# Optimization experiments

Measured on AMD Instinct MI355X. Metric: run time of the kernel, lower is better.

Reference implementation:

```python
import jax, jax.numpy as jnp
import numpy as np

B, K, V = 64, 8, 128000
PLACEHOLDER = -1


def setup_inputs() -> dict:
    key = jax.random.key(0)
    k1, k2, k3, k4, k5 = jax.random.split(key, 5)
    draft_token_ids = jax.random.randint(k1, (B, K), 0, V, dtype=jnp.int32)
    # normalized probability distributions, as the kernel expects
    draft_probs = jax.nn.softmax(jax.random.normal(k2, (B, K, V), dtype=jnp.float32), axis=-1)
    target_probs = jax.nn.softmax(jax.random.normal(k3, (B, K, V), dtype=jnp.float32), axis=-1)
    bonus_token_ids = jax.random.randint(k4, (B,), 0, V, dtype=jnp.int32)
    uniform_samples = jax.random.uniform(k5, (B, K), dtype=jnp.float32)
    return {
        "draft_token_ids": draft_token_ids,
        "draft_probs": draft_probs,
        "target_probs": target_probs,
        "bonus_token_ids": bonus_token_ids,
        "uniform_samples": uniform_samples,
    }


def reference(draft_token_ids, draft_probs, target_probs, bonus_token_ids, uniform_samples):
    """Speculative-decoding rejection sampling (dense layout, all requests have K drafts).

    Returns (output_token_ids [B,K+1] int32, num_accepted, accepted_counts,
             recovered_counts, bonus_counts) matching RejectionSampleOutput.
    """
    b_idx = jnp.arange(B)
    # gather p(t), q(t) at the drafted token ids: [B, K]
    p = jnp.take_along_axis(target_probs, draft_token_ids[..., None].astype(jnp.int32), axis=-1)[..., 0]
    q = jnp.take_along_axis(draft_probs, draft_token_ids[..., None].astype(jnp.int32), axis=-1)[..., 0]
    accept_prob = jnp.minimum(1.0, p / jnp.maximum(q, 1e-10))
    accept = uniform_samples < accept_prob                      # [B, K] bool
    # number of leading accepted tokens (sequential accept/reject chain)
    prefix = jnp.cumprod(accept.astype(jnp.int32), axis=1)
    num_acc = jnp.sum(prefix, axis=1)                           # [B]
    all_acc = num_acc == K
    # first rejected position (clamped for the all-accepted case)
    j = jnp.minimum(num_acc, K - 1)
    tgt_j = target_probs[b_idx, j]                              # [B, V]
    drf_j = draft_probs[b_idx, j]                               # [B, V]
    # recovery distribution: normalized max(p - q, 0); sample via inverse-CDF
    res = jnp.maximum(tgt_j - drf_j, 0.0)
    cdf = jnp.cumsum(res, axis=-1)                              # [B, V]
    total = cdf[:, -1]
    u_j = uniform_samples[b_idx, j]
    recovered = jnp.argmax(cdf > (u_j * total)[:, None], axis=-1)
    recovered = jnp.where(total > 0, recovered, jnp.argmax(tgt_j, axis=-1)).astype(jnp.int32)
    # last emitted token: bonus if everything accepted, else recovered
    last = jnp.where(all_acc, bonus_token_ids, recovered)       # [B]
    pos = jnp.arange(K + 1)[None, :]                            # [1, K+1]
    draft_pad = jnp.pad(draft_token_ids, ((0, 0), (0, 1)))      # [B, K+1]
    out = jnp.where(pos < num_acc[:, None], draft_pad,
                    jnp.where(pos == num_acc[:, None], last[:, None], PLACEHOLDER))
    accepted_counts = num_acc.astype(jnp.int32)
    recovered_counts = (1 - all_acc.astype(jnp.int32))
    bonus_counts = all_acc.astype(jnp.int32)
    return (out.astype(jnp.int32), num_acc.astype(jnp.int32), accepted_counts,
            recovered_counts, bonus_counts)
```

## Files before the change

### kernel.cpp

```cpp
#include <hip/hip_runtime.h>

#define BB 64
#define KK 8
#define VV 128000
#define TILE 1024
#define NTILES 125
#define SPLIT 8
#define TPS 16
#define NWAVES 8
#define PLACEHOLDER (-1)

#define WS_TSUM 0
#define WS_AV   (BB * NTILES)
#define WS_AI   (WS_AV + BB * SPLIT * NWAVES)
#define WS_NA   (WS_AI + BB * SPLIT * NWAVES)

__device__ __forceinline__ int accept_na(const int* __restrict__ draft_ids,
                                         const float* __restrict__ draft_probs,
                                         const float* __restrict__ target_probs,
                                         const float* __restrict__ uniforms, int b) {
    int   ids[KK];
    float us[KK], ps[KK], qs[KK];
#pragma unroll
    for (int k = 0; k < KK; ++k) ids[k] = draft_ids[b * KK + k];
#pragma unroll
    for (int k = 0; k < KK; ++k) us[k] = uniforms[b * KK + k];
#pragma unroll
    for (int k = 0; k < KK; ++k) {
        long r = (long)(b * KK + k) * VV + ids[k];
        ps[k]  = target_probs[r];
        qs[k]  = draft_probs[r];
    }
    int  na  = 0;
    bool run = true;
#pragma unroll
    for (int k = 0; k < KK; ++k) {
        bool acc = us[k] < fminf(1.0f, ps[k] / fmaxf(qs[k], 1e-10f));
        run      = run && acc;
        na += run ? 1 : 0;
    }
    return na;
}

__global__ __launch_bounds__(512) void pass_a_kernel(
    const int* __restrict__ draft_ids, const float* __restrict__ draft_probs,
    const float* __restrict__ target_probs, const float* __restrict__ uniforms,
    float* __restrict__ ws_f, int* __restrict__ ws_i) {
    const int s    = blockIdx.x;
    const int b    = blockIdx.y;
    const int tid  = threadIdx.x;
    const int lane = tid & 63;
    const int w    = tid >> 6;

    int na = accept_na(draft_ids, draft_probs, target_probs, uniforms, b);
    if (s == 0 && tid == 0) ws_i[WS_NA + b] = na;
    if (na == KK) return;
    int j = na < (KK - 1) ? na : (KK - 1);

    const float* __restrict__ tgt = target_probs + (long)(b * KK + j) * VV;
    const float* __restrict__ drf = draft_probs + (long)(b * KK + j) * VV;

    float mval = -1.0f;
    int   midx = 0;
    const int t0 = s * TPS;
#pragma unroll
    for (int i = 0; i < 2; ++i) {
        int t = t0 + w + NWAVES * i;
        if (t >= NTILES) continue;
        float ssum = 0.0f;
#pragma unroll
        for (int g = 0; g < 4; ++g) {
            int    off = t * TILE + g * 256 + lane * 4;
            float4 tv  = *(const float4*)(tgt + off);
            float4 dv  = *(const float4*)(drf + off);
            ssum += fmaxf(tv.x - dv.x, 0.0f) + fmaxf(tv.y - dv.y, 0.0f) +
                    fmaxf(tv.z - dv.z, 0.0f) + fmaxf(tv.w - dv.w, 0.0f);
            if (tv.x > mval) { mval = tv.x; midx = off; }
            if (tv.y > mval) { mval = tv.y; midx = off + 1; }
            if (tv.z > mval) { mval = tv.z; midx = off + 2; }
            if (tv.w > mval) { mval = tv.w; midx = off + 3; }
        }
        for (int o = 32; o > 0; o >>= 1) ssum += __shfl_xor(ssum, o, 64);
        if (lane == 0) ws_f[WS_TSUM + b * NTILES + t] = ssum;
    }
    for (int o = 32; o > 0; o >>= 1) {
        float ov = __shfl_xor(mval, o, 64);
        int   oi = __shfl_xor(midx, o, 64);
        if (ov > mval || (ov == mval && oi < midx)) { mval = ov; midx = oi; }
    }
    if (lane == 0) {
        ws_f[WS_AV + b * SPLIT * NWAVES + s * NWAVES + w] = mval;
        ws_i[WS_AI + b * SPLIT * NWAVES + s * NWAVES + w] = midx;
    }
}

__global__ __launch_bounds__(64) void finalize_kernel(
    const int* __restrict__ draft_ids, const float* __restrict__ draft_probs,
    const float* __restrict__ target_probs, const int* __restrict__ bonus_ids,
    const float* __restrict__ uniforms, const float* __restrict__ ws_f,
    const int* __restrict__ ws_i, int* __restrict__ out) {
    const int b    = blockIdx.x;
    const int lane = threadIdx.x;

    __shared__ float s_ts[NTILES];
    __shared__ float s_total, s_thr, s_P;
    __shared__ int   s_ct;

    float ts0 = ws_f[WS_TSUM + b * NTILES + lane];
    float ts1 = 0.0f;
    if (lane < NTILES - 64) ts1 = ws_f[WS_TSUM + b * NTILES + lane + 64];

    int na  = ws_i[WS_NA + b];
    int all = (na == KK) ? 1 : 0;
    int j   = na < (KK - 1) ? na : (KK - 1);

    if (lane <= KK) {
        bool wr = true;
        int  v;
        if (lane < na) v = draft_ids[b * KK + lane];
        else if (lane == na) { if (all) v = bonus_ids[b]; else wr = false; }
        else v = PLACEHOLDER;
        if (wr) out[b * (KK + 1) + lane] = v;
    }
    if (lane == 0) {
        out[BB * (KK + 1) + b]          = na;
        out[BB * (KK + 1) + BB + b]     = na;
        out[BB * (KK + 1) + 2 * BB + b] = 1 - all;
        out[BB * (KK + 1) + 3 * BB + b] = all;
    }
    if (all) return;

    s_ts[lane] = ts0;
    if (lane < NTILES - 64) s_ts[lane + 64] = ts1;
    __syncthreads();

    if (lane == 0) {
        float u_j   = uniforms[b * KK + j];
        float total = 0.0f;
        for (int t = 0; t < NTILES; ++t) total += s_ts[t];
        float thr = u_j * total;
        float run = 0.0f;
        int   ct  = -1;
        float P   = 0.0f;
        for (int t = 0; t < NTILES; ++t) {
            if (run + s_ts[t] > thr) { ct = t; P = run; break; }
            run += s_ts[t];
        }
        s_total = total; s_thr = thr; s_P = P; s_ct = ct;
    }
    __syncthreads();

    const float total = s_total, thr = s_thr, P = s_P;
    const int   ct    = s_ct;
    int rec;
    if (total > 0.0f) {
        if (ct < 0) {
            rec = VV - 1;
        } else {
            const float* __restrict__ tgt = target_probs + (long)(b * KK + j) * VV;
            const float* __restrict__ drf = draft_probs + (long)(b * KK + j) * VV;
            float G     = 0.0f;
            int   cand  = 0x7fffffff;
            int   tbase = ct * TILE;
#pragma unroll
            for (int g = 0; g < 4; ++g) {
                int    off = tbase + g * 256 + lane * 4;
                float4 tv  = *(const float4*)(tgt + off);
                float4 dv  = *(const float4*)(drf + off);
                float  r0  = fmaxf(tv.x - dv.x, 0.0f);
                float  r1  = fmaxf(tv.y - dv.y, 0.0f);
                float  r2  = fmaxf(tv.z - dv.z, 0.0f);
                float  r3  = fmaxf(tv.w - dv.w, 0.0f);
                float  ls  = r0 + r1 + r2 + r3;
                float  inc = ls;
                for (int o = 1; o < 64; o <<= 1) {
                    float n = __shfl_up(inc, o, 64);
                    if (lane >= o) inc += n;
                }
                float lex  = inc - ls;
                float runp = P + G + lex;
                float p0 = runp + r0, p1 = p0 + r1, p2 = p1 + r2, p3 = p2 + r3;
                int   c  = 0x7fffffff;
                if (p3 > thr) c = off + 3;
                if (p2 > thr) c = off + 2;
                if (p1 > thr) c = off + 1;
                if (p0 > thr) c = off;
                cand = min(cand, c);
                G += __shfl(inc, 63, 64);
            }
            for (int o = 32; o > 0; o >>= 1) cand = min(cand, __shfl_xor(cand, o, 64));
            rec = (cand == 0x7fffffff) ? (tbase + TILE - 1) : cand;
        }
    } else {
        float v = ws_f[WS_AV + b * SPLIT * NWAVES + lane];
        int   i = ws_i[WS_AI + b * SPLIT * NWAVES + lane];
        for (int o = 32; o > 0; o >>= 1) {
            float ov = __shfl_xor(v, o, 64);
            int   oi = __shfl_xor(i, o, 64);
            if (ov > v || (ov == v && oi < i)) { v = ov; i = oi; }
        }
        rec = i;
    }
    if (lane == 0) out[b * (KK + 1) + na] = rec;
}

extern "C" void kernel_launch(void* const* d_in, const int* in_sizes, int n_in,
                              void* d_out, int out_size, void* d_ws, size_t ws_size,
                              hipStream_t stream) {
    const int*   draft_ids    = (const int*)d_in[0];
    const float* draft_probs  = (const float*)d_in[1];
    const float* target_probs = (const float*)d_in[2];
    const int*   bonus_ids    = (const int*)d_in[3];
    const float* uniforms     = (const float*)d_in[4];
    int*         out          = (int*)d_out;
    float*       ws_f         = (float*)d_ws;
    int*         ws_i         = (int*)d_ws;

    pass_a_kernel<<<dim3(SPLIT, BB), 512, 0, stream>>>(draft_ids, draft_probs,
                                                       target_probs, uniforms, ws_f, ws_i);
    finalize_kernel<<<BB, 64, 0, stream>>>(draft_ids, draft_probs, target_probs,
                                           bonus_ids, uniforms, ws_f, ws_i, out);
}
```

Before: 419.1 us.

## Fuse pass-A and finalize into one cooperative kernel with grid sync

Merges the two kernel launches into one cooperative launch of 512 blocks, using a grid-wide sync between the partial-sum/argmax pass and the per-row finalize step. Block 0 of each row then does the CDF search and writes outputs. The aim is to remove the second launch overhead and inter-kernel gap. In exchange it pays for a cooperative grid barrier and needs all 512 blocks of 512 threads to be co-resident. Blocks whose row has every draft accepted no longer exit early, because they must reach the barrier.

```diff
diff --git a/kernel.cpp b/kernel.cpp
--- a/kernel.cpp
+++ b/kernel.cpp
@@ -1,4 +1,7 @@
 #include <hip/hip_runtime.h>
+#include <hip/hip_cooperative_groups.h>
+
+namespace cg = cooperative_groups;
 
 #define BB 64
 #define KK 8
@@ -13,7 +16,6 @@
 #define WS_TSUM 0
 #define WS_AV   (BB * NTILES)
 #define WS_AI   (WS_AV + BB * SPLIT * NWAVES)
-#define WS_NA   (WS_AI + BB * SPLIT * NWAVES)
 
 __device__ __forceinline__ int accept_na(const int* __restrict__ draft_ids,
                                          const float* __restrict__ draft_probs,
@@ -42,87 +44,79 @@
     return na;
 }
 
-__global__ __launch_bounds__(512) void pass_a_kernel(
+__global__ __launch_bounds__(512) void fused_kernel(
     const int* __restrict__ draft_ids, const float* __restrict__ draft_probs,
-    const float* __restrict__ target_probs, const float* __restrict__ uniforms,
-    float* __restrict__ ws_f, int* __restrict__ ws_i) {
+    const float* __restrict__ target_probs, const int* __restrict__ bonus_ids,
+    const float* __restrict__ uniforms, float* __restrict__ ws_f,
+    int* __restrict__ ws_i, int* __restrict__ out) {
     const int s    = blockIdx.x;
     const int b    = blockIdx.y;
     const int tid  = threadIdx.x;
     const int lane = tid & 63;
     const int w    = tid >> 6;
 
-    int na = accept_na(draft_ids, draft_probs, target_probs, uniforms, b);
-    if (s == 0 && tid == 0) ws_i[WS_NA + b] = na;
-    if (na == KK) return;
-    int j = na < (KK - 1) ? na : (KK - 1);
+    int na  = accept_na(draft_ids, draft_probs, target_probs, uniforms, b);
+    int all = (na == KK) ? 1 : 0;
+    int j   = na < (KK - 1) ? na : (KK - 1);
 
     const float* __restrict__ tgt = target_probs + (long)(b * KK + j) * VV;
     const float* __restrict__ drf = draft_probs + (long)(b * KK + j) * VV;
 
-    float mval = -1.0f;
-    int   midx = 0;
-    const int t0 = s * TPS;
-#pragma unroll
-    for (int i = 0; i < 2; ++i) {
-        int t = t0 + w + NWAVES * i;
-        if (t >= NTILES) continue;
-        float ssum = 0.0f;
-#pragma unroll
-        for (int g = 0; g < 4; ++g) {
-            int    off = t * TILE + g * 256 + lane * 4;
-            float4 tv  = *(const float4*)(tgt + off);
-            float4 dv  = *(const float4*)(drf + off);
-            ssum += fmaxf(tv.x - dv.x, 0.0f) + fmaxf(tv.y - dv.y, 0.0f) +
-                    fmaxf(tv.z - dv.z, 0.0f) + fmaxf(tv.w - dv.w, 0.0f);
-            if (tv.x > mval) { mval = tv.x; midx = off; }
-            if (tv.y > mval) { mval = tv.y; midx = off + 1; }
-            if (tv.z > mval) { mval = tv.z; midx = off + 2; }
-            if (tv.w > mval) { mval = tv.w; midx = off + 3; }
-        }
-        for (int o = 32; o > 0; o >>= 1) ssum += __shfl_xor(ssum, o, 64);
-        if (lane == 0) ws_f[WS_TSUM + b * NTILES + t] = ssum;
-    }
-    for (int o = 32; o > 0; o >>= 1) {
-        float ov = __shfl_xor(mval, o, 64);
-        int   oi = __shfl_xor(midx, o, 64);
-        if (ov > mval || (ov == mval && oi < midx)) { mval = ov; midx = oi; }
-    }
-    if (lane == 0) {
-        ws_f[WS_AV + b * SPLIT * NWAVES + s * NWAVES + w] = mval;
-        ws_i[WS_AI + b * SPLIT * NWAVES + s * NWAVES + w] = midx;
-    }
-}
-
-__global__ __launch_bounds__(64) void finalize_kernel(
-    const int* __restrict__ draft_ids, const float* __restrict__ draft_probs,
-    const float* __restrict__ target_probs, const int* __restrict__ bonus_ids,
-    const float* __restrict__ uniforms, const float* __restrict__ ws_f,
-    const int* __restrict__ ws_i, int* __restrict__ out) {
-    const int b    = blockIdx.x;
-    const int lane = threadIdx.x;
+    if (!all) {
+        float mval = -1.0f;
+        int   midx = 0;
+        const int t0 = s * TPS;
+#pragma unroll
+        for (int i = 0; i < 2; ++i) {
+            int t = t0 + w + NWAVES * i;
+            if (t >= NTILES) continue;
+            float ssum = 0.0f;
+#pragma unroll
+            for (int g = 0; g < 4; ++g) {
+                int    off = t * TILE + g * 256 + lane * 4;
+                float4 tv  = *(const float4*)(tgt + off);
+                float4 dv  = *(const float4*)(drf + off);
+                ssum += fmaxf(tv.x - dv.x, 0.0f) + fmaxf(tv.y - dv.y, 0.0f) +
+                        fmaxf(tv.z - dv.z, 0.0f) + fmaxf(tv.w - dv.w, 0.0f);
+                if (tv.x > mval) { mval = tv.x; midx = off; }
+                if (tv.y > mval) { mval = tv.y; midx = off + 1; }
+                if (tv.z > mval) { mval = tv.z; midx = off + 2; }
+                if (tv.w > mval) { mval = tv.w; midx = off + 3; }
+            }
+            for (int o = 32; o > 0; o >>= 1) ssum += __shfl_xor(ssum, o, 64);
+            if (lane == 0) ws_f[WS_TSUM + b * NTILES + t] = ssum;
+        }
+        for (int o = 32; o > 0; o >>= 1) {
+            float ov = __shfl_xor(mval, o, 64);
+            int   oi = __shfl_xor(midx, o, 64);
+            if (ov > mval || (ov == mval && oi < midx)) { mval = ov; midx = oi; }
+        }
+        if (lane == 0) {
+            ws_f[WS_AV + b * SPLIT * NWAVES + s * NWAVES + w] = mval;
+            ws_i[WS_AI + b * SPLIT * NWAVES + s * NWAVES + w] = midx;
+        }
+    }
+    __threadfence();
+    cg::this_grid().sync();
+
+    if (s != 0) return;
 
     __shared__ float s_ts[NTILES];
     __shared__ float s_total, s_thr, s_P;
     __shared__ int   s_ct;
 
-    float ts0 = ws_f[WS_TSUM + b * NTILES + lane];
-    float ts1 = 0.0f;
-    if (lane < NTILES - 64) ts1 = ws_f[WS_TSUM + b * NTILES + lane + 64];
-
-    int na  = ws_i[WS_NA + b];
-    int all = (na == KK) ? 1 : 0;
-    int j   = na < (KK - 1) ? na : (KK - 1);
-
-    if (lane <= KK) {
+    float tsv = 0.0f;
+    if (tid < NTILES) tsv = ws_f[WS_TSUM + b * NTILES + tid];
+
+    if (tid <= KK) {
         bool wr = true;
         int  v;
-        if (lane < na) v = draft_ids[b * KK + lane];
-        else if (lane == na) { if (all) v = bonus_ids[b]; else wr = false; }
+        if (tid < na) v = draft_ids[b * KK + tid];
+        else if (tid == na) { if (all) v = bonus_ids[b]; else wr = false; }
         else v = PLACEHOLDER;
-        if (wr) out[b * (KK + 1) + lane] = v;
-    }
-    if (lane == 0) {
+        if (wr) out[b * (KK + 1) + tid] = v;
+    }
+    if (tid == 0) {
         out[BB * (KK + 1) + b]          = na;
         out[BB * (KK + 1) + BB + b]     = na;
         out[BB * (KK + 1) + 2 * BB + b] = 1 - all;
@@ -130,11 +124,10 @@
     }
     if (all) return;
 
-    s_ts[lane] = ts0;
-    if (lane < NTILES - 64) s_ts[lane + 64] = ts1;
+    if (tid < NTILES) s_ts[tid] = tsv;
     __syncthreads();
 
-    if (lane == 0) {
+    if (tid == 0) {
         float u_j   = uniforms[b * KK + j];
         float total = 0.0f;
         for (int t = 0; t < NTILES; ++t) total += s_ts[t];
@@ -150,6 +143,8 @@
     }
     __syncthreads();
 
+    if (tid >= 64) return;
+
     const float total = s_total, thr = s_thr, P = s_P;
     const int   ct    = s_ct;
     int rec;
@@ -157,8 +152,6 @@
         if (ct < 0) {
             rec = VV - 1;
         } else {
-            const float* __restrict__ tgt = target_probs + (long)(b * KK + j) * VV;
-            const float* __restrict__ drf = draft_probs + (long)(b * KK + j) * VV;
             float G     = 0.0f;
             int   cand  = 0x7fffffff;
             int   tbase = ct * TILE;
@@ -216,8 +209,9 @@
     float*       ws_f         = (float*)d_ws;
     int*         ws_i         = (int*)d_ws;
 
-    pass_a_kernel<<<dim3(SPLIT, BB), 512, 0, stream>>>(draft_ids, draft_probs,
-                                                       target_probs, uniforms, ws_f, ws_i);
-    finalize_kernel<<<BB, 64, 0, stream>>>(draft_ids, draft_probs, target_probs,
-                                           bonus_ids, uniforms, ws_f, ws_i, out);
+    void* args[] = {(void*)&draft_ids, (void*)&draft_probs, (void*)&target_probs,
+                    (void*)&bonus_ids, (void*)&uniforms, (void*)&ws_f,
+                    (void*)&ws_i, (void*)&out};
+    hipLaunchCooperativeKernel((void*)fused_kernel, dim3(SPLIT, BB), dim3(512),
+                               args, 0, stream);
 }
```

After: 633.7 us. +51.2%, slower.
